# Kernel tuning notes

Measured on AMD Instinct MI355X. Metric: run time of the kernel, lower is better.

The kernel has to match this reference:

```python
import jax, jax.numpy as jnp
import numpy as np

T_MAX = 201  # TEXT_MAX_LEN
HID = 512
VOCAB = 100  # NUM_CHAR
BATCH = 2048


def setup_inputs() -> dict:
    key = jax.random.key(0)
    ks = jax.random.split(key, 8)
    s = 0.05  # keep gates in a sane range
    return {
        "feat": jax.random.normal(ks[0], (BATCH, HID), jnp.float32),      # resnet pooler_output
        "W_ih": jax.random.normal(ks[1], (3 * HID, HID), jnp.float32) * s,  # torch weight_ih_l0 (r,z,n)
        "W_hh": jax.random.normal(ks[2], (3 * HID, HID), jnp.float32) * s,
        "b_ih": jax.random.normal(ks[3], (3 * HID,), jnp.float32) * s,
        "b_hh": jax.random.normal(ks[4], (3 * HID,), jnp.float32) * s,
        "W_proj": jax.random.normal(ks[5], (VOCAB, HID), jnp.float32) * s,
        "b_proj": jax.random.normal(ks[6], (VOCAB,), jnp.float32) * s,
        "embed": jax.random.normal(ks[7], (VOCAB, HID), jnp.float32) * s,
        "sos": 0,
    }


def _gru_cell(x, h, W_ih, W_hh, b_ih, b_hh):
    # torch GRU cell: gates ordered (reset, update, new)
    gi = x @ W_ih.T + b_ih            # [B, 3H]
    gh = h @ W_hh.T + b_hh            # [B, 3H]
    i_r, i_z, i_n = jnp.split(gi, 3, axis=-1)
    h_r, h_z, h_n = jnp.split(gh, 3, axis=-1)
    r = jax.nn.sigmoid(i_r + h_r)
    z = jax.nn.sigmoid(i_z + h_z)
    n = jnp.tanh(i_n + r * h_n)
    return (1.0 - z) * n + z * h


def reference(feat, W_ih, W_hh, b_ih, b_hh, W_proj, b_proj, embed, sos):
    B = feat.shape[0]
    # start token embedding broadcast over batch
    x0 = jnp.broadcast_to(embed[sos], (B, HID))
    h0 = feat  # encoder features initialize the GRU hidden state

    def step(carry, _):
        h, x = carry
        h = _gru_cell(x, h, W_ih, W_hh, b_ih, b_hh)
        logits = h @ W_proj.T + b_proj          # [B, V]
        pred = jnp.argmax(logits, axis=-1)      # greedy decode
        x_next = embed[pred]                    # [B, H]
        return (h, x_next), logits

    _, logits_tbv = jax.lax.scan(step, (h0, x0), None, length=T_MAX)  # [T, B, V]
    # outputs.permute(0, 2, 1): [B, V, T]
    return jnp.transpose(logits_tbv, (1, 2, 0))
```

## Files before the change

kernel.cpp:

```cpp
#include <hip/hip_runtime.h>
#include <cmath>

#define HID   512
#define VOCAB 100
#define G3    1536
#define GEXT  1664
#define NT    104
#define TMAX  201
#define ROWS  8
#define BLOCK 1024
#define NWG   256
#define TPW   13
#define GHS   1672

typedef __bf16 bf16x8 __attribute__((ext_vector_type(8)));
typedef float  f32x4  __attribute__((ext_vector_type(4)));

#define SZ_WPK   (NT * 16 * 2 * 64 * 8)
#define FBASE    (SZ_WPK / 2)
#define OFF_EIH  FBASE
#define SZ_EIH   (VOCAB * G3)
#define OFF_WIHT (OFF_EIH + SZ_EIH)
#define SZ_WIHT  (HID * G3)
#define OFF_BEXT (OFF_WIHT + SZ_WIHT)

__global__ void prep_kernel(const float* __restrict__ W_ih,
                            const float* __restrict__ b_hh,
                            const float* __restrict__ b_proj,
                            float* __restrict__ ws)
{
  int idx = blockIdx.x * 256 + threadIdx.x;
  if (idx < SZ_WIHT) {
    int k = idx / G3, j = idx - k * G3;
    ws[OFF_WIHT + idx] = W_ih[j * HID + k];
  } else if (idx < SZ_WIHT + GEXT) {
    int j = idx - SZ_WIHT;
    float v = 0.f;
    if (j < G3)              v = b_hh[j];
    else if (j < G3 + VOCAB) v = b_proj[j - G3];
    ws[OFF_BEXT + j] = v;
  }
}

__global__ void pack_kernel(const float* __restrict__ W_hh,
                            const float* __restrict__ W_proj,
                            __bf16* __restrict__ wpk)
{
  int idx = blockIdx.x * 256 + threadIdx.x;
  if (idx >= NT * 16 * 64 * 8) return;
  int j    = idx & 7;
  int lane = (idx >> 3) & 63;
  int ks   = (idx >> 9) & 15;
  int c    = idx >> 13;
  int col  = c * 16 + (lane & 15);
  int k    = ks * 32 + (lane >> 4) * 8 + j;
  float w = 0.f;
  if (col < G3)              w = W_hh[col * HID + k];
  else if (col < G3 + VOCAB) w = W_proj[(col - G3) * HID + k];
  __bf16 hi = (__bf16)w;
  __bf16 lo = (__bf16)(w - (float)hi);
  int base = (((c * 16 + ks) * 2) * 64 + lane) * 8 + j;
  wpk[base]       = hi;
  wpk[base + 512] = lo;
}

__global__ void eih_kernel(const float* __restrict__ embed,
                           const float* __restrict__ b_ih,
                           float* __restrict__ ws)
{
  int v = blockIdx.x / 6;
  int j = (blockIdx.x % 6) * 256 + threadIdx.x;
  const float* WihT = ws + OFF_WIHT;
  const float* e = embed + v * HID;
  float acc = b_ih[j];
  for (int k = 0; k < HID; ++k)
    acc = fmaf(WihT[k * G3 + j], e[k], acc);
  ws[OFF_EIH + v * G3 + j] = acc;
}

__global__ __launch_bounds__(BLOCK) void decode_kernel(
    const float* __restrict__ feat,
    const int* __restrict__ sos,
    const float* __restrict__ ws,
    const __bf16* __restrict__ wpk,
    float* __restrict__ out)
{
  __shared__ __align__(16) char hab[16 * 1024];
  __shared__ float ghA[ROWS][GHS];
  __shared__ float ghB[ROWS][GHS];
  __shared__ int   pred_lds[ROWS];

  const float* __restrict__ EIH  = ws + OFF_EIH;
  const float* __restrict__ bext = ws + OFF_BEXT;

  const int tid  = threadIdx.x;
  const int lane = tid & 63;
  const int wv   = tid >> 6;
  const int half = wv >> 3;
  const int wt   = wv & 7;
  const int b0   = blockIdx.x * ROWS;
  const int u    = tid & (HID - 1);
  const int rb   = (tid >> 9) * 4;

  float (*ghW)[GHS] = half ? ghB : ghA;

  float h[4];
  #pragma unroll
  for (int rr = 0; rr < 4; ++rr) {
    int r = rb + rr;
    float f = feat[(size_t)(b0 + r) * HID + u];
    h[rr] = f;
    __bf16 hi = (__bf16)f;
    __bf16 lo = (__bf16)(f - (float)hi);
    unsigned so = ((unsigned)(u * 2)) ^ (((unsigned)(r & 7)) << 4);
    *(__bf16*)(hab + (r << 10) + so)       = hi;
    *(__bf16*)(hab + ((r + 8) << 10) + so) = lo;
  }
  if (tid < ROWS) pred_lds[tid] = sos[0];
  __syncthreads();

  const float gbr = bext[u], gbz = bext[HID + u], gbn = bext[2 * HID + u];
  const int sr = tid / VOCAB, sv = tid - sr * VOCAB;
  float* outp = nullptr; float outb = 0.f;
  if (tid < ROWS * VOCAB) {
    outp = out + ((size_t)(b0 + sr) * VOCAB + sv) * TMAX;
    outb = bext[G3 + sv];
  }
  const float ab0 = (lane < VOCAB)      ? bext[G3 + lane]      : 0.f;
  const float ab1 = (lane + 64 < VOCAB) ? bext[G3 + 64 + lane] : 0.f;

  const int      arow = lane & 15;
  const unsigned ag   = (unsigned)((lane >> 4) << 4);
  const unsigned axor = ((unsigned)(arow & 7)) << 4;
  const char* ha = hab + (arow << 10);

  for (int t = 0; t <= TMAX; ++t) {
    bf16x8 afr[8];
    #pragma unroll
    for (int q = 0; q < 8; ++q) {
      int ks = half * 8 + q;
      afr[q] = *(const bf16x8*)(ha + ((((unsigned)ks << 6) + ag) ^ axor));
    }

    for (int tt = 0; tt < TPW; ++tt) {
      int tile = wt * TPW + tt;
      if (t == TMAX && tile < 96) continue;
      f32x4 acc = {0.f, 0.f, 0.f, 0.f};
      const bf16x8* bp = ((const bf16x8*)wpk)
                         + (size_t)tile * 2048 + (size_t)half * 1024 + lane;
      #pragma unroll
      for (int q = 0; q < 8; ++q) {
        bf16x8 bh = bp[q * 128];
        bf16x8 bl = bp[q * 128 + 64];
        acc = __builtin_amdgcn_mfma_f32_16x16x32_bf16(afr[q], bh, acc, 0, 0, 0);
        acc = __builtin_amdgcn_mfma_f32_16x16x32_bf16(afr[q], bl, acc, 0, 0, 0);
      }
      int colw = tile * 16 + (lane & 15);
      float vs[4];
      #pragma unroll
      for (int i = 0; i < 4; ++i)
        vs[i] = acc[i] + __shfl_xor(acc[i], 32, 64);
      if (lane < 32) {
        int r0 = (lane >> 4) * 4;
        #pragma unroll
        for (int i = 0; i < 4; ++i)
          ghW[r0 + i][colw] = vs[i];
      }
    }
    __syncthreads();

    if (t >= 1) {
      if (tid < ROWS * VOCAB) {
        float lg = ghA[sr][G3 + sv] + ghB[sr][G3 + sv] + outb;
        __builtin_nontemporal_store(lg, outp + (t - 1));
      }
      if (t < TMAX && wv < ROWS) {
        float v0 = (lane < VOCAB)
                   ? ghA[wv][G3 + lane] + ghB[wv][G3 + lane] + ab0 : -1e30f;
        float v1 = (lane + 64 < VOCAB)
                   ? ghA[wv][G3 + 64 + lane] + ghB[wv][G3 + 64 + lane] + ab1 : -1e30f;
        float bv; int bi;
        if (v0 >= v1) { bv = v0; bi = lane; } else { bv = v1; bi = lane + 64; }
        #pragma unroll
        for (int off = 32; off >= 1; off >>= 1) {
          float ov = __shfl_xor(bv, off);
          int   oi = __shfl_xor(bi, off);
          if (ov > bv || (ov == bv && oi < bi)) { bv = ov; bi = oi; }
        }
        if (lane == 0) pred_lds[wv] = bi;
      }
    }
    __syncthreads();

    if (t < TMAX) {
      #pragma unroll
      for (int rr = 0; rr < 4; ++rr) {
        int r = rb + rr;
        const float* eb = EIH + (size_t)pred_lds[r] * G3;
        float srg = eb[u]       + gbr + ghA[r][u]       + ghB[r][u];
        float szg = eb[HID + u] + gbz + ghA[r][HID + u] + ghB[r][HID + u];
        float hn  = ghA[r][2 * HID + u] + ghB[r][2 * HID + u] + gbn;
        float rg = 1.f / (1.f + expf(-srg));
        float zg = 1.f / (1.f + expf(-szg));
        float ng = tanhf(eb[2 * HID + u] + rg * hn);
        h[rr] = (1.f - zg) * ng + zg * h[rr];
        __bf16 hi = (__bf16)h[rr];
        __bf16 lo = (__bf16)(h[rr] - (float)hi);
        unsigned so = ((unsigned)(u * 2)) ^ (((unsigned)(r & 7)) << 4);
        *(__bf16*)(hab + (r << 10) + so)       = hi;
        *(__bf16*)(hab + ((r + 8) << 10) + so) = lo;
      }
    }
    __syncthreads();
  }
}

extern "C" void kernel_launch(void* const* d_in, const int* in_sizes, int n_in,
                              void* d_out, int out_size, void* d_ws, size_t ws_size,
                              hipStream_t stream)
{
  const float* feat   = (const float*)d_in[0];
  const float* W_ih   = (const float*)d_in[1];
  const float* W_hh   = (const float*)d_in[2];
  const float* b_ih   = (const float*)d_in[3];
  const float* b_hh   = (const float*)d_in[4];
  const float* W_proj = (const float*)d_in[5];
  const float* b_proj = (const float*)d_in[6];
  const float* embed  = (const float*)d_in[7];
  const int*   sos    = (const int*)d_in[8];

  float*  wsf = (float*)d_ws;
  __bf16* wpk = (__bf16*)d_ws;
  float*  out = (float*)d_out;

  const int prep_total = SZ_WIHT + GEXT;
  prep_kernel<<<(prep_total + 255) / 256, 256, 0, stream>>>(W_ih, b_hh, b_proj, wsf);
  pack_kernel<<<(NT * 16 * 64 * 8 + 255) / 256, 256, 0, stream>>>(W_hh, W_proj, wpk);
  eih_kernel<<<600, 256, 0, stream>>>(embed, b_ih, wsf);
  decode_kernel<<<NWG, BLOCK, 0, stream>>>(feat, sos, wsf, wpk, out);
}
```

Baseline: 6.631 ms.

## Software-pipeline weight loads with inline asm double buffering and explicit vmcnt waits

Replaces the compiler-scheduled per-tile weight loads with inline-asm global_load_dwordx4 groups. Two register sets alternate, so the next chunk's loads are issued before the current chunk's MFMAs, and s_waitcnt vmcnt plus sched_barrier enforce the order. This also prefetches across tile boundaries to hide global memory latency in the recurrent GEMV. The final-step skip is rewritten so only the wave owning the projection tiles runs. It adds register pressure, and asm volatile limits the compiler's own scheduling.

```diff
diff --git a/kernel.cpp b/kernel.cpp
--- a/kernel.cpp
+++ b/kernel.cpp
@@ -15,6 +15,7 @@
 
 typedef __bf16 bf16x8 __attribute__((ext_vector_type(8)));
 typedef float  f32x4  __attribute__((ext_vector_type(4)));
+typedef unsigned int u32x4 __attribute__((ext_vector_type(4)));
 
 #define SZ_WPK   (NT * 16 * 2 * 64 * 8)
 #define FBASE    (SZ_WPK / 2)
@@ -78,6 +79,43 @@
   ws[OFF_EIH + v * G3 + j] = acc;
 }
 
+#define GLD4(F0, F1, F2, F3, P)                                   \
+  asm volatile("global_load_dwordx4 %0, %4, off\n\t"              \
+               "global_load_dwordx4 %1, %4, off offset:1024\n\t"  \
+               "global_load_dwordx4 %2, %4, off offset:2048\n\t"  \
+               "global_load_dwordx4 %3, %4, off offset:3072"      \
+               : "=&v"(F0), "=&v"(F1), "=&v"(F2), "=&v"(F3)       \
+               : "v"(P))
+
+#define VMWAIT(N)                                 \
+  do { asm volatile("s_waitcnt vmcnt(" #N ")");   \
+       __builtin_amdgcn_sched_barrier(0); } while (0)
+
+#define BC(X) __builtin_bit_cast(bf16x8, X)
+
+#define MFMA4(ACC, Q0, Q1, Q2, Q3, A0, A1)                                      \
+  do {                                                                          \
+    ACC = __builtin_amdgcn_mfma_f32_16x16x32_bf16(A0, BC(Q0), ACC, 0, 0, 0);    \
+    ACC = __builtin_amdgcn_mfma_f32_16x16x32_bf16(A0, BC(Q1), ACC, 0, 0, 0);    \
+    ACC = __builtin_amdgcn_mfma_f32_16x16x32_bf16(A1, BC(Q2), ACC, 0, 0, 0);    \
+    ACC = __builtin_amdgcn_mfma_f32_16x16x32_bf16(A1, BC(Q3), ACC, 0, 0, 0);    \
+  } while (0)
+
+#define FOLDWRITE(ACC, TILE)                                      \
+  do {                                                            \
+    int colw_ = (TILE) * 16 + (lane & 15);                        \
+    float vs_[4];                                                 \
+    _Pragma("unroll")                                             \
+    for (int i_ = 0; i_ < 4; ++i_)                                \
+      vs_[i_] = ACC[i_] + __shfl_xor(ACC[i_], 32, 64);            \
+    if (lane < 32) {                                              \
+      int r0_ = (lane >> 4) * 4;                                  \
+      _Pragma("unroll")                                           \
+      for (int i_ = 0; i_ < 4; ++i_)                              \
+        ghW[r0_ + i_][colw_] = vs_[i_];                           \
+    }                                                             \
+  } while (0)
+
 __global__ __launch_bounds__(BLOCK) void decode_kernel(
     const float* __restrict__ feat,
     const int* __restrict__ sos,
@@ -134,37 +172,54 @@
   const unsigned axor = ((unsigned)(arow & 7)) << 4;
   const char* ha = hab + (arow << 10);
 
+  const char* const wbase = (const char*)wpk
+      + (size_t)(wt * TPW) * 32768 + (size_t)half * 16384 + (size_t)lane * 16;
+
   for (int t = 0; t <= TMAX; ++t) {
-    bf16x8 afr[8];
-    #pragma unroll
-    for (int q = 0; q < 8; ++q) {
-      int ks = half * 8 + q;
-      afr[q] = *(const bf16x8*)(ha + ((((unsigned)ks << 6) + ag) ^ axor));
-    }
-
-    for (int tt = 0; tt < TPW; ++tt) {
-      int tile = wt * TPW + tt;
-      if (t == TMAX && tile < 96) continue;
-      f32x4 acc = {0.f, 0.f, 0.f, 0.f};
-      const bf16x8* bp = ((const bf16x8*)wpk)
-                         + (size_t)tile * 2048 + (size_t)half * 1024 + lane;
-      #pragma unroll
-      for (int q = 0; q < 8; ++q) {
-        bf16x8 bh = bp[q * 128];
-        bf16x8 bl = bp[q * 128 + 64];
-        acc = __builtin_amdgcn_mfma_f32_16x16x32_bf16(afr[q], bh, acc, 0, 0, 0);
-        acc = __builtin_amdgcn_mfma_f32_16x16x32_bf16(afr[q], bl, acc, 0, 0, 0);
-      }
-      int colw = tile * 16 + (lane & 15);
-      float vs[4];
-      #pragma unroll
-      for (int i = 0; i < 4; ++i)
-        vs[i] = acc[i] + __shfl_xor(acc[i], 32, 64);
-      if (lane < 32) {
-        int r0 = (lane >> 4) * 4;
-        #pragma unroll
-        for (int i = 0; i < 4; ++i)
-          ghW[r0 + i][colw] = vs[i];
+    bf16x8 afr0, afr1, afr2, afr3, afr4, afr5, afr6, afr7;
+    {
+      const unsigned kb = (unsigned)(half * 8);
+      afr0 = *(const bf16x8*)(ha + ((((kb + 0) << 6) + ag) ^ axor));
+      afr1 = *(const bf16x8*)(ha + ((((kb + 1) << 6) + ag) ^ axor));
+      afr2 = *(const bf16x8*)(ha + ((((kb + 2) << 6) + ag) ^ axor));
+      afr3 = *(const bf16x8*)(ha + ((((kb + 3) << 6) + ag) ^ axor));
+      afr4 = *(const bf16x8*)(ha + ((((kb + 4) << 6) + ag) ^ axor));
+      afr5 = *(const bf16x8*)(ha + ((((kb + 5) << 6) + ag) ^ axor));
+      afr6 = *(const bf16x8*)(ha + ((((kb + 6) << 6) + ag) ^ axor));
+      afr7 = *(const bf16x8*)(ha + ((((kb + 7) << 6) + ag) ^ axor));
+    }
+
+    int tt0 = 0;
+    bool active = true;
+    if (t == TMAX) { if (wt == 7) tt0 = 5; else active = false; }
+
+    if (active) {
+      u32x4 qa0, qa1, qa2, qa3;
+      u32x4 qb0, qb1, qb2, qb3;
+      const char* bp = wbase + (size_t)tt0 * 32768;
+
+      GLD4(qa0, qa1, qa2, qa3, bp);
+
+      for (int tt = tt0; tt < TPW; ++tt) {
+        f32x4 acc = {0.f, 0.f, 0.f, 0.f};
+        GLD4(qb0, qb1, qb2, qb3, bp + 4096);
+        VMWAIT(4);
+        MFMA4(acc, qa0, qa1, qa2, qa3, afr0, afr1);
+        GLD4(qa0, qa1, qa2, qa3, bp + 8192);
+        VMWAIT(4);
+        MFMA4(acc, qb0, qb1, qb2, qb3, afr2, afr3);
+        GLD4(qb0, qb1, qb2, qb3, bp + 12288);
+        VMWAIT(4);
+        MFMA4(acc, qa0, qa1, qa2, qa3, afr4, afr5);
+        if (tt + 1 < TPW) {
+          GLD4(qa0, qa1, qa2, qa3, bp + 32768);
+          VMWAIT(4);
+        } else {
+          VMWAIT(0);
+        }
+        MFMA4(acc, qb0, qb1, qb2, qb3, afr6, afr7);
+        FOLDWRITE(acc, wt * TPW + tt);
+        bp += 32768;
       }
     }
     __syncthreads();
```

After: 6.347 ms. -4.3%, faster.
